# Kernel optimization log

Measured on AMD Instinct MI355X. Metric: run time of the kernel, lower is better.

Reference implementation:

```python
import jax, jax.numpy as jnp
import numpy as np

B, N, D = 8, 1024, 768
H = 12
HD = D // H  # 64
SCALE = HD ** -0.5


def setup_inputs() -> dict:
    key = jax.random.key(0)
    k1, k2, k3 = jax.random.split(key, 3)
    x = jax.random.normal(k1, (B, N, D), dtype=jnp.float32)
    qkv_w = jax.random.normal(k2, (3 * D, D), dtype=jnp.float32) * 0.02
    proj_w = jax.random.normal(k3, (D, D), dtype=jnp.float32) * 0.02
    proj_b = jnp.zeros((D,), dtype=jnp.float32)
    return {"x": x, "qkv_w": qkv_w, "proj_w": proj_w, "proj_b": proj_b}


def reference(x, qkv_w, proj_w, proj_b):
    # qkv projection: [B,N,3D] -> [3,B,H,N,HD]
    qkv = jnp.einsum('bnd,ed->bne', x, qkv_w)
    qkv = qkv.reshape(B, N, 3, H, HD).transpose(2, 0, 3, 1, 4)
    q, k, v = qkv[0], qkv[1], qkv[2]
    # scaled dot-product attention
    attn = jnp.einsum('bhqd,bhkd->bhqk', q * SCALE, k)
    attn = jax.nn.softmax(attn, axis=-1)
    out = jnp.einsum('bhqk,bhkd->bhqd', attn, v)
    out = out.transpose(0, 2, 1, 3).reshape(B, N, D)
    # output projection
    return jnp.einsum('bnd,ed->bne', out, proj_w) + proj_b
```

## Files before the change

### kernel.cpp

```cpp
#include <hip/hip_runtime.h>

typedef unsigned short ushort;
typedef __attribute__((ext_vector_type(4)))  float  f32x4;
typedef __attribute__((ext_vector_type(16))) float  f32x16;
typedef __attribute__((ext_vector_type(8)))  short  s16x8;
typedef __attribute__((ext_vector_type(4)))  ushort u16x4;
typedef __attribute__((ext_vector_type(4)))  unsigned u32x4;

#define MFMA16(a, b, c) __builtin_amdgcn_mfma_f32_16x16x32_bf16((a), (b), (c), 0, 0, 0)
#define MFMA32(a, b, c) __builtin_amdgcn_mfma_f32_32x32x16_bf16((a), (b), (c), 0, 0, 0)

__device__ __forceinline__ ushort f2bf(float f) {
    unsigned u = __builtin_bit_cast(unsigned, f);
    u = (u + 0x7FFF + ((u >> 16) & 1)) >> 16;
    return (ushort)u;
}

__device__ __forceinline__ unsigned cvtpk_bf16(float lo, float hi) {
    unsigned r;
    asm("v_cvt_pk_bf16_f32 %0, %1, %2" : "=v"(r) : "v"(lo), "v"(hi));
    return r;
}
__device__ __forceinline__ void plswap(unsigned& a, unsigned& b) {
    asm volatile("v_permlane32_swap_b32 %0, %1" : "+v"(a), "+v"(b));
}
__device__ __forceinline__ float pairmax(float x) {
    return fmaxf(x, __shfl_xor(x, 32));
}
__device__ __forceinline__ float pairsum(float x) {
    return x + __shfl_xor(x, 32);
}
__device__ __forceinline__ float fast_exp2(float x) {
    float r;
    asm("v_exp_f32 %0, %1" : "=v"(r) : "v"(x));
    return r;
}

__device__ __forceinline__ void gload_lds16(const ushort* g, ushort* l) {
    __builtin_amdgcn_global_load_lds(
        (const __attribute__((address_space(1))) void*)g,
        (__attribute__((address_space(3))) void*)l, 16, 0, 0);
}

__global__ __launch_bounds__(256) void cvt_f32_bf16(
    const float* __restrict__ in, ushort* __restrict__ out, int n4)
{
    int i = blockIdx.x * blockDim.x + threadIdx.x;
    const int stride = gridDim.x * blockDim.x;
    for (; i < n4; i += stride) {
        const float4 v = ((const float4*)in)[i];
        u16x4 o;
        o[0] = f2bf(v.x); o[1] = f2bf(v.y); o[2] = f2bf(v.z); o[3] = f2bf(v.w);
        ((u16x4*)out)[i] = o;
    }
}

__device__ __forceinline__ void gemm128_mainloop(
    const ushort* __restrict__ A, const ushort* __restrict__ B, int K,
    int row0, int col0, ushort* As, ushort* Bs, f32x4 acc[4][4])
{
    const int t  = threadIdx.x;
    const int l  = t & 63;
    const int w  = t >> 6;
    const int lr = l & 15, lg = l >> 4;
    const int wm = w >> 1, wn = w & 1;

#pragma unroll
    for (int m = 0; m < 4; m++)
#pragma unroll
        for (int n = 0; n < 4; n++) acc[m][n] = (f32x4){0.f, 0.f, 0.f, 0.f};

    const ushort* ga0 = A + (row0 + (t >> 2)) * K + (t & 3) * 8;
    const ushort* gb0 = B + (col0 + (t >> 2)) * K + (t & 3) * 8;
    ushort* la0 = As + t * 8;
    ushort* lb0 = Bs + t * 8;
    const int rowsz = 64 * K;

    for (int k0 = 0; k0 < K; k0 += 32) {
        gload_lds16(ga0 + k0,          la0);
        gload_lds16(ga0 + rowsz + k0,  la0 + 2048);
        gload_lds16(gb0 + k0,          lb0);
        gload_lds16(gb0 + rowsz + k0,  lb0 + 2048);
        __syncthreads();

        s16x8 af[4], bfr[4];
#pragma unroll
        for (int m = 0; m < 4; m++)
            af[m] = *(const s16x8*)&As[(wm * 64 + m * 16 + lr) * 32 + lg * 8];
#pragma unroll
        for (int n = 0; n < 4; n++)
            bfr[n] = *(const s16x8*)&Bs[(wn * 64 + n * 16 + lr) * 32 + lg * 8];
#pragma unroll
        for (int m = 0; m < 4; m++)
#pragma unroll
            for (int n = 0; n < 4; n++)
                acc[m][n] = MFMA16(af[m], bfr[n], acc[m][n]);
        __syncthreads();
    }
}

__global__ __launch_bounds__(256) void qkv_gemm(
    const ushort* __restrict__ X, const ushort* __restrict__ W,
    ushort* __restrict__ qb, ushort* __restrict__ kb, ushort* __restrict__ vb)
{
    __shared__ __align__(16) ushort As[128 * 32];
    __shared__ __align__(16) ushort Bs[128 * 32];
    f32x4 acc[4][4];
    const int br = blockIdx.x, bc = blockIdx.y;
    gemm128_mainloop(X, W, 768, br * 128, bc * 128, As, Bs, acc);

    const int t = threadIdx.x, l = t & 63, w = t >> 6;
    const int lr = l & 15, lg = l >> 4, wm = w >> 1, wn = w & 1;
    const int p = (bc * 128) / 768;
    const int mrow0 = br * 128 + wm * 64 + lg * 4;
    const int ecolB = bc * 128 + wn * 64 + lr;
    const float QSCALE = 0.125f * 1.44269504088896f;

#pragma unroll
    for (int n = 0; n < 4; n++) {
        const int e   = ecolB + n * 16;
        const int rem = e - p * 768;
        const int h   = rem >> 6;
        const int hd  = rem & 63;
#pragma unroll
        for (int m = 0; m < 4; m++) {
            const int mr = mrow0 + m * 16;
            const int b  = mr >> 10;
            const int nn = mr & 1023;
            const f32x4 v = acc[m][n];
            const int bh = b * 12 + h;
            if (p == 0) {
                ushort* dst = qb + (bh * 1024 + nn) * 64 + hd;
#pragma unroll
                for (int r = 0; r < 4; r++) dst[r * 64] = f2bf(v[r] * QSCALE);
            } else if (p == 1) {
                ushort* dst = kb + (bh * 1024 + nn) * 64 + hd;
#pragma unroll
                for (int r = 0; r < 4; r++) dst[r * 64] = f2bf(v[r]);
            } else {
                u16x4 pk;
                pk[0] = f2bf(v[0]); pk[1] = f2bf(v[1]);
                pk[2] = f2bf(v[2]); pk[3] = f2bf(v[3]);
                *(u16x4*)(vb + (bh * 64 + hd) * 1024 + nn) = pk;
            }
        }
    }
}

__global__ __launch_bounds__(256) void attn_kernel(
    const ushort* __restrict__ qb, const ushort* __restrict__ kb,
    const ushort* __restrict__ vb, ushort* __restrict__ ao)
{
    __shared__ __align__(16) ushort KV[2][4096];
    const int bh = blockIdx.x, qt = blockIdx.y;
    const int b = bh / 12, h = bh - b * 12;
    const int t = threadIdx.x, l = t & 63, w = t >> 6;
    const int lq = l & 31, hi = l >> 5;
    const int qr0 = qt * 128 + w * 32;

    const int l3 = l >> 3, l7 = l & 7;
    const int ku = w * 8 + l3;
    const int pfv = l7 ^ l3;
    const char* ksrc = (const char*)kb + (size_t)(bh * 1024 + ku) * 128
                     + ((l7 ^ l3) << 4);
    const char* vsrc = (const char*)vb + (size_t)(bh * 64 + ku + 32 * ((pfv >> 2) & 1)) * 2048
                     + ((pfv & 3) << 4);
    ushort* kdst = &KV[0][0]    + w * 512 + l * 8;
    ushort* vdst = &KV[0][2048] + w * 512 + l * 8;

    const ushort* qlane = qb + (bh * 1024 + qr0 + lq) * 64 + hi * 8;
    s16x8 qf[4];
#pragma unroll
    for (int s = 0; s < 4; s++) qf[s] = *(const s16x8*)(qlane + s * 16);

    float m = -__builtin_inff();
    float lsum = 0.f;
    f32x16 o0 = {}, o1 = {};

    gload_lds16((const ushort*)ksrc, kdst);
    gload_lds16((const ushort*)vsrc, vdst);
    __syncthreads();

    const int fx = (lq & 7) << 4;
    for (int it = 0; it < 32; ++it) {
        const int cur = it & 1;
        if (it < 31) {
            const int kvn = (it + 1) * 32;
            gload_lds16((const ushort*)(ksrc + kvn * 128), kdst + (cur ^ 1) * 4096);
            gload_lds16((const ushort*)(vsrc + kvn * 2),   vdst + (cur ^ 1) * 4096);
        }
        const char* Kb = (const char*)&KV[cur][0];
        const char* Vb = (const char*)&KV[cur][2048];

        s16x8 kf[4];
#pragma unroll
        for (int s = 0; s < 4; s++)
            kf[s] = *(const s16x8*)(Kb + lq * 128 + ((hi * 16 + s * 32) ^ fx));

        f32x16 sa = {};
        __builtin_amdgcn_s_setprio(1);
#pragma unroll
        for (int s = 0; s < 4; s++) sa = MFMA32(kf[s], qf[s], sa);
        __builtin_amdgcn_s_setprio(0);

        float tm[8];
#pragma unroll
        for (int r = 0; r < 8; r++) tm[r] = fmaxf(sa[r], sa[r + 8]);
#pragma unroll
        for (int s = 4; s; s >>= 1)
#pragma unroll
            for (int r = 0; r < s; r++) tm[r] = fmaxf(tm[r], tm[r + s]);
        const float mx = pairmax(tm[0]);

        if (!__all(mx <= m + 8.f)) {
            const float mn = fmaxf(m, mx);
            const float fac = fast_exp2(m - mn);
            m = mn;
            lsum *= fac;
#pragma unroll
            for (int r = 0; r < 16; r++) { o0[r] *= fac; o1[r] *= fac; }
        }

        float p[16];
#pragma unroll
        for (int r = 0; r < 16; r++) p[r] = fast_exp2(sa[r] - m);
        float ts[8];
#pragma unroll
        for (int r = 0; r < 8; r++) ts[r] = p[r] + p[r + 8];
#pragma unroll
        for (int s = 4; s; s >>= 1)
#pragma unroll
            for (int r = 0; r < s; r++) ts[r] += ts[r + s];
        lsum += pairsum(ts[0]);

        s16x8 pfr[2];
#pragma unroll
        for (int slot = 0; slot < 2; slot++) {
            const int r0 = slot * 8;
            unsigned a0 = cvtpk_bf16(p[r0 + 0], p[r0 + 1]);
            unsigned a1 = cvtpk_bf16(p[r0 + 4], p[r0 + 5]);
            plswap(a0, a1);
            unsigned b0 = cvtpk_bf16(p[r0 + 2], p[r0 + 3]);
            unsigned b1 = cvtpk_bf16(p[r0 + 6], p[r0 + 7]);
            plswap(b0, b1);
            const u32x4 u = {a0, b0, a1, b1};
            pfr[slot] = __builtin_bit_cast(s16x8, u);
        }

        s16x8 vf[2][2];
#pragma unroll
        for (int half = 0; half < 2; half++)
#pragma unroll
            for (int s = 0; s < 2; s++)
                vf[half][s] = *(const s16x8*)(Vb + lq * 128 + ((half * 64 + hi * 16 + s * 32) ^ fx));
        __builtin_amdgcn_s_setprio(1);
        o0 = MFMA32(vf[0][0], pfr[0], o0);
        o1 = MFMA32(vf[1][0], pfr[0], o1);
        o0 = MFMA32(vf[0][1], pfr[1], o0);
        o1 = MFMA32(vf[1][1], pfr[1], o1);
        __builtin_amdgcn_s_setprio(0);

        __syncthreads();
    }

    const float inv = 1.f / lsum;
    ushort* op = ao + (b * 1024 + qr0 + lq) * 768 + h * 64 + 4 * hi;
#pragma unroll
    for (int i = 0; i < 4; i++) {
        u16x4 pk0, pk1;
#pragma unroll
        for (int j = 0; j < 4; j++) {
            pk0[j] = f2bf(o0[4 * i + j] * inv);
            pk1[j] = f2bf(o1[4 * i + j] * inv);
        }
        *(u16x4*)(op + 8 * i)      = pk0;
        *(u16x4*)(op + 32 + 8 * i) = pk1;
    }
}

__global__ __launch_bounds__(256) void proj_gemm(
    const ushort* __restrict__ A, const ushort* __restrict__ W,
    const float* __restrict__ bias, float* __restrict__ out)
{
    __shared__ __align__(16) ushort As[128 * 32];
    __shared__ __align__(16) ushort Bs[128 * 32];
    f32x4 acc[4][4];
    const int br = blockIdx.x, bc = blockIdx.y;
    gemm128_mainloop(A, W, 768, br * 128, bc * 128, As, Bs, acc);

    const int t = threadIdx.x, l = t & 63, w = t >> 6;
    const int lr = l & 15, lg = l >> 4, wm = w >> 1, wn = w & 1;
    const int mrow0 = br * 128 + wm * 64 + lg * 4;
    const int ecolB = bc * 128 + wn * 64 + lr;

#pragma unroll
    for (int n = 0; n < 4; n++) {
        const int e = ecolB + n * 16;
        const float bv = bias[e];
#pragma unroll
        for (int m = 0; m < 4; m++) {
            const int mr = mrow0 + m * 16;
#pragma unroll
            for (int r = 0; r < 4; r++)
                out[(mr + r) * 768 + e] = acc[m][n][r] + bv;
        }
    }
}

extern "C" void kernel_launch(void* const* d_in, const int* in_sizes, int n_in,
                              void* d_out, int out_size, void* d_ws, size_t ws_size,
                              hipStream_t stream)
{
    const float* x  = (const float*)d_in[0];
    const float* wq = (const float*)d_in[1];
    const float* wp = (const float*)d_in[2];
    const float* pb = (const float*)d_in[3];
    float* out = (float*)d_out;

    const int NX = 8 * 1024 * 768;
    const int NQ = 2304 * 768;
    const int NP = 768 * 768;
    const int SEG = 8 * 12 * 1024 * 64;

    ushort* xb  = (ushort*)d_ws;
    ushort* wqb = xb + NX;
    ushort* wpb = wqb + NQ;
    ushort* qb  = wpb + NP;
    ushort* kb  = qb + SEG;
    ushort* vb  = kb + SEG;
    ushort* ao  = xb;

    cvt_f32_bf16<<<2048, 256, 0, stream>>>(x,  xb,  NX / 4);
    cvt_f32_bf16<<<1024, 256, 0, stream>>>(wq, wqb, NQ / 4);
    cvt_f32_bf16<<<576,  256, 0, stream>>>(wp, wpb, NP / 4);

    qkv_gemm  <<<dim3(64, 18), 256, 0, stream>>>(xb, wqb, qb, kb, vb);
    attn_kernel<<<dim3(96, 8), 256, 0, stream>>>(qb, kb, vb, ao);
    proj_gemm <<<dim3(64, 6),  256, 0, stream>>>(ao, wpb, pb, out);
}
```

Baseline: 132.8 us.

## Double-buffer LDS tiles in GEMM mainloop and raise MFMA wave priority

The shared GEMM mainloop used by the QKV and output projection kernels now uses two LDS buffers. It issues the global-to-LDS loads for the next K-slice before computing on the current one, so load latency overlaps with MFMA work. It also wraps the MFMA block in s_setprio to favour math issue. This doubles LDS per block, which may lower occupancy. Correctness relies on the async global-to-LDS loads having completed by the single barrier at the end of each iteration.

```diff
diff --git a/kernel.cpp b/kernel.cpp
--- a/kernel.cpp
+++ b/kernel.cpp
@@ -72,29 +72,44 @@
 
     const ushort* ga0 = A + (row0 + (t >> 2)) * K + (t & 3) * 8;
     const ushort* gb0 = B + (col0 + (t >> 2)) * K + (t & 3) * 8;
+    const int rowsz = 64 * K;
     ushort* la0 = As + t * 8;
     ushort* lb0 = Bs + t * 8;
-    const int rowsz = 64 * K;
-
-    for (int k0 = 0; k0 < K; k0 += 32) {
-        gload_lds16(ga0 + k0,          la0);
-        gload_lds16(ga0 + rowsz + k0,  la0 + 2048);
-        gload_lds16(gb0 + k0,          lb0);
-        gload_lds16(gb0 + rowsz + k0,  lb0 + 2048);
-        __syncthreads();
+
+    gload_lds16(ga0,         la0);
+    gload_lds16(ga0 + rowsz, la0 + 2048);
+    gload_lds16(gb0,         lb0);
+    gload_lds16(gb0 + rowsz, lb0 + 2048);
+    __syncthreads();
+
+    const int nt = K >> 5;
+    for (int it = 0; it < nt; ++it) {
+        const int cur = it & 1;
+        if (it + 1 < nt) {
+            const int k0  = (it + 1) * 32;
+            const int nxt = (cur ^ 1) * 4096;
+            gload_lds16(ga0 + k0,         la0 + nxt);
+            gload_lds16(ga0 + rowsz + k0, la0 + nxt + 2048);
+            gload_lds16(gb0 + k0,         lb0 + nxt);
+            gload_lds16(gb0 + rowsz + k0, lb0 + nxt + 2048);
+        }
+        const ushort* Ab = As + cur * 4096;
+        const ushort* Bb = Bs + cur * 4096;
 
         s16x8 af[4], bfr[4];
 #pragma unroll
         for (int m = 0; m < 4; m++)
-            af[m] = *(const s16x8*)&As[(wm * 64 + m * 16 + lr) * 32 + lg * 8];
+            af[m] = *(const s16x8*)&Ab[(wm * 64 + m * 16 + lr) * 32 + lg * 8];
 #pragma unroll
         for (int n = 0; n < 4; n++)
-            bfr[n] = *(const s16x8*)&Bs[(wn * 64 + n * 16 + lr) * 32 + lg * 8];
+            bfr[n] = *(const s16x8*)&Bb[(wn * 64 + n * 16 + lr) * 32 + lg * 8];
+        __builtin_amdgcn_s_setprio(1);
 #pragma unroll
         for (int m = 0; m < 4; m++)
 #pragma unroll
             for (int n = 0; n < 4; n++)
                 acc[m][n] = MFMA16(af[m], bfr[n], acc[m][n]);
+        __builtin_amdgcn_s_setprio(0);
         __syncthreads();
     }
 }
@@ -103,8 +118,8 @@
     const ushort* __restrict__ X, const ushort* __restrict__ W,
     ushort* __restrict__ qb, ushort* __restrict__ kb, ushort* __restrict__ vb)
 {
-    __shared__ __align__(16) ushort As[128 * 32];
-    __shared__ __align__(16) ushort Bs[128 * 32];
+    __shared__ __align__(16) ushort As[2 * 128 * 32];
+    __shared__ __align__(16) ushort Bs[2 * 128 * 32];
     f32x4 acc[4][4];
     const int br = blockIdx.x, bc = blockIdx.y;
     gemm128_mainloop(X, W, 768, br * 128, bc * 128, As, Bs, acc);
@@ -282,8 +297,8 @@
     const ushort* __restrict__ A, const ushort* __restrict__ W,
     const float* __restrict__ bias, float* __restrict__ out)
 {
-    __shared__ __align__(16) ushort As[128 * 32];
-    __shared__ __align__(16) ushort Bs[128 * 32];
+    __shared__ __align__(16) ushort As[2 * 128 * 32];
+    __shared__ __align__(16) ushort Bs[2 * 128 * 32];
     f32x4 acc[4][4];
     const int br = blockIdx.x, bc = blockIdx.y;
     gemm128_mainloop(A, W, 768, br * 128, bc * 128, As, Bs, acc);
```

Result: faster. 128.4 us (-3.3%).

## Triple-buffer LDS in shared GEMM mainloop to overlap loads with MFMA

Applied to the files above, without the earlier changes.

Replaces the single-buffered load-sync-compute-sync loop in the shared 128x128 GEMM mainloop with a three-stage ring of LDS buffers. Tiles are prefetched two steps ahead using direct global-to-LDS loads, with vmcnt waits and a single barrier per step. It also raises wave priority around the MFMA block. The aim is to hide global load latency behind matrix math in both the QKV and output projection GEMMs, at the cost of triple the LDS per block, which may reduce occupancy.

```diff
diff --git a/kernel.cpp b/kernel.cpp
--- a/kernel.cpp
+++ b/kernel.cpp
@@ -72,39 +72,68 @@
 
     const ushort* ga0 = A + (row0 + (t >> 2)) * K + (t & 3) * 8;
     const ushort* gb0 = B + (col0 + (t >> 2)) * K + (t & 3) * 8;
+    const int rowsz = 64 * K;
     ushort* la0 = As + t * 8;
     ushort* lb0 = Bs + t * 8;
-    const int rowsz = 64 * K;
-
-    for (int k0 = 0; k0 < K; k0 += 32) {
-        gload_lds16(ga0 + k0,          la0);
-        gload_lds16(ga0 + rowsz + k0,  la0 + 2048);
-        gload_lds16(gb0 + k0,          lb0);
-        gload_lds16(gb0 + rowsz + k0,  lb0 + 2048);
-        __syncthreads();
-
+
+    auto STAGE = [&](int kt, int buf) {
+        const int k0  = kt * 32;
+        const int off = buf * 4096;
+        gload_lds16(ga0 + k0,         la0 + off);
+        gload_lds16(ga0 + rowsz + k0, la0 + off + 2048);
+        gload_lds16(gb0 + k0,         lb0 + off);
+        gload_lds16(gb0 + rowsz + k0, lb0 + off + 2048);
+    };
+    auto COMPUTE = [&](int buf) {
+        const ushort* Ab = As + buf * 4096;
+        const ushort* Bb = Bs + buf * 4096;
         s16x8 af[4], bfr[4];
 #pragma unroll
         for (int m = 0; m < 4; m++)
-            af[m] = *(const s16x8*)&As[(wm * 64 + m * 16 + lr) * 32 + lg * 8];
+            af[m] = *(const s16x8*)&Ab[(wm * 64 + m * 16 + lr) * 32 + lg * 8];
 #pragma unroll
         for (int n = 0; n < 4; n++)
-            bfr[n] = *(const s16x8*)&Bs[(wn * 64 + n * 16 + lr) * 32 + lg * 8];
+            bfr[n] = *(const s16x8*)&Bb[(wn * 64 + n * 16 + lr) * 32 + lg * 8];
+        __builtin_amdgcn_s_setprio(1);
 #pragma unroll
         for (int m = 0; m < 4; m++)
 #pragma unroll
             for (int n = 0; n < 4; n++)
                 acc[m][n] = MFMA16(af[m], bfr[n], acc[m][n]);
-        __syncthreads();
-    }
+        __builtin_amdgcn_s_setprio(0);
+    };
+
+    const int nt = K >> 5;
+    STAGE(0, 0);
+    STAGE(1, 1);
+    asm volatile("s_waitcnt vmcnt(4)" ::: "memory");
+    __builtin_amdgcn_s_barrier();
+
+#define GSTEP(IT, CBUF, SBUF)                                          \
+    {                                                                  \
+        const int sk = (IT) + 2;                                       \
+        const bool st = sk < nt;                                       \
+        if (st) STAGE(sk, SBUF);                                       \
+        COMPUTE(CBUF);                                                 \
+        if (st) { asm volatile("s_waitcnt vmcnt(4)" ::: "memory"); }   \
+        else    { asm volatile("s_waitcnt vmcnt(0)" ::: "memory"); }   \
+        __builtin_amdgcn_s_barrier();                                  \
+    }
+
+    for (int base = 0; base < nt; base += 3) {
+        GSTEP(base,     0, 2);
+        GSTEP(base + 1, 1, 0);
+        GSTEP(base + 2, 2, 1);
+    }
+#undef GSTEP
 }
 
 __global__ __launch_bounds__(256) void qkv_gemm(
     const ushort* __restrict__ X, const ushort* __restrict__ W,
     ushort* __restrict__ qb, ushort* __restrict__ kb, ushort* __restrict__ vb)
 {
-    __shared__ __align__(16) ushort As[128 * 32];
-    __shared__ __align__(16) ushort Bs[128 * 32];
+    __shared__ __align__(16) ushort As[3 * 128 * 32];
+    __shared__ __align__(16) ushort Bs[3 * 128 * 32];
     f32x4 acc[4][4];
     const int br = blockIdx.x, bc = blockIdx.y;
     gemm128_mainloop(X, W, 768, br * 128, bc * 128, As, Bs, acc);
@@ -282,8 +311,8 @@
     const ushort* __restrict__ A, const ushort* __restrict__ W,
     const float* __restrict__ bias, float* __restrict__ out)
 {
-    __shared__ __align__(16) ushort As[128 * 32];
-    __shared__ __align__(16) ushort Bs[128 * 32];
+    __shared__ __align__(16) ushort As[3 * 128 * 32];
+    __shared__ __align__(16) ushort Bs[3 * 128 * 32];
     f32x4 acc[4][4];
     const int br = blockIdx.x, bc = blockIdx.y;
     gemm128_mainloop(A, W, 768, br * 128, bc * 128, As, Bs, acc);
```

New measurement: 120.8 us. 9.0% less time.
